# Performance work log

Hardware: AMD Instinct MI355X
Metric: run time of the kernel (lower is better)

The kernel has to match this reference:

```python
import jax, jax.numpy as jnp
import numpy as np


def setup_inputs() -> dict:
    key = jax.random.key(0)
    T, B, N = 2048, 16, 2048
    spikes = (jax.random.uniform(key, (T, B, N)) < 0.05).astype(jnp.float32)
    return {"input_spikes": spikes, "duration": 100}


def reference(input_spikes, duration):
    # Causal sliding-window (boxcar) sum over the time axis of length `duration`,
    # equivalent to conv1d with a ones kernel and causal padding, then clamp to [0,1].
    # psp[t] = clip( sum_{k=max(0,t-duration+1)}^{t} x[k], 0, 1 )
    T = input_spikes.shape[0]
    c = jnp.cumsum(input_spikes, axis=0)                     # [T, ...]
    pad = [(duration, 0)] + [(0, 0)] * (input_spikes.ndim - 1)
    c_shift = jnp.pad(c, pad)[:T]                            # c[t-duration], 0 for t<duration
    win = c - c_shift
    return jnp.clip(win, 0.0, 1.0)
```

## Files before the change

### kernel.cpp

```cpp
#include <hip/hip_runtime.h>


#define T_TOTAL 2048
#define M_COLS  (16 * 2048)
#define CHUNK   256
#define VEC     2
#define BATCH   8

typedef float v2f __attribute__((ext_vector_type(2)));

__device__ __forceinline__ void loadb(v2f (&dst)[BATCH], const v2f* __restrict__ xc,
                                      int tb, int stride) {
    #pragma unroll
    for (int i = 0; i < BATCH; ++i) dst[i] = xc[(tb + i) * stride];
}

__device__ __forceinline__ void procb(const v2f (&v)[BATCH], v2f* __restrict__ oc,
                                      int tb, int stride, int t0, int duration,
                                      int& last0, int& last1) {
    #pragma unroll
    for (int i = 0; i < BATCH; ++i) {
        const int tt = tb + i;
        if (v[i].x != 0.0f) last0 = tt;
        if (v[i].y != 0.0f) last1 = tt;
        if (tt >= t0) {
            v2f o;
            o.x = (tt - last0 < duration) ? 1.0f : 0.0f;
            o.y = (tt - last1 < duration) ? 1.0f : 0.0f;
            __builtin_nontemporal_store(o, &oc[tt * stride]);
        }
    }
}

__global__ __launch_bounds__(256, 1) void psp_scan_kernel(
    const float* __restrict__ x,
    const int*  __restrict__ dur_p,
    float* __restrict__ out)
{
    const int pair = blockIdx.x * blockDim.x + threadIdx.x;
    const int col  = pair * VEC;
    const int t0   = blockIdx.y * CHUNK;
    const int duration = dur_p[0];

    int hal = (duration - 1 + (BATCH - 1)) & ~(BATCH - 1);
    if (hal > t0) hal = t0;
    const int tstart = t0 - hal;
    const int NB = (hal + CHUNK) / BATCH;

    int last0 = tstart - duration;
    int last1 = last0;

    const v2f* __restrict__ xc = (const v2f*)(x + col);
    v2f* __restrict__ oc       = (v2f*)(out + col);
    const int stride = M_COLS / VEC;

    v2f va[BATCH], vb[BATCH];

    int t = tstart;
    loadb(va, xc, t, stride);

    int b = 0;
    while (b + 2 <= NB) {
        loadb(vb, xc, t + BATCH, stride);
        __builtin_amdgcn_sched_barrier(0);
        procb(va, oc, t, stride, t0, duration, last0, last1);

        if (b + 2 < NB) loadb(va, xc, t + 2 * BATCH, stride);
        __builtin_amdgcn_sched_barrier(0);
        procb(vb, oc, t + BATCH, stride, t0, duration, last0, last1);

        t += 2 * BATCH;
        b += 2;
    }
    if (b < NB) {
        procb(va, oc, t, stride, t0, duration, last0, last1);
    }
}

extern "C" void kernel_launch(void* const* d_in, const int* in_sizes, int n_in,
                              void* d_out, int out_size, void* d_ws, size_t ws_size,
                              hipStream_t stream) {
    const float* x     = (const float*)d_in[0];
    const int*   dur_p = (const int*)d_in[1];
    float*       out   = (float*)d_out;

    dim3 grid(M_COLS / VEC / 256, T_TOTAL / CHUNK);
    dim3 block(256);
    psp_scan_kernel<<<grid, block, 0, stream>>>(x, dur_p, out);
}
```

Measured before the change: 465.8 us.

## Halve time chunk, raise occupancy, replace double-buffering with inline-asm batched loads

Halves the time chunk per block, which doubles the grid, and raises launch bounds to allow 4 blocks per CU. Latency is meant to be hidden by occupancy instead of the software double-buffer, which is replaced by simple batched inline-asm loads followed by a full vmcnt wait. The halo warm-up is split into a separate loop without stores. Smaller chunks increase the relative halo reread overhead (about 104 extra rows per 128), adding memory traffic.

```diff
diff --git a/kernel.cpp b/kernel.cpp
--- a/kernel.cpp
+++ b/kernel.cpp
@@ -3,36 +3,16 @@
 
 #define T_TOTAL 2048
 #define M_COLS  (16 * 2048)
-#define CHUNK   256
+#define CHUNK   128
 #define VEC     2
 #define BATCH   8
 
 typedef float v2f __attribute__((ext_vector_type(2)));
 
-__device__ __forceinline__ void loadb(v2f (&dst)[BATCH], const v2f* __restrict__ xc,
-                                      int tb, int stride) {
-    #pragma unroll
-    for (int i = 0; i < BATCH; ++i) dst[i] = xc[(tb + i) * stride];
-}
+#define GLOAD2(dst, ptr) \
+    asm volatile("global_load_dwordx2 %0, %1, off" : "=v"(dst) : "v"(ptr))
 
-__device__ __forceinline__ void procb(const v2f (&v)[BATCH], v2f* __restrict__ oc,
-                                      int tb, int stride, int t0, int duration,
-                                      int& last0, int& last1) {
-    #pragma unroll
-    for (int i = 0; i < BATCH; ++i) {
-        const int tt = tb + i;
-        if (v[i].x != 0.0f) last0 = tt;
-        if (v[i].y != 0.0f) last1 = tt;
-        if (tt >= t0) {
-            v2f o;
-            o.x = (tt - last0 < duration) ? 1.0f : 0.0f;
-            o.y = (tt - last1 < duration) ? 1.0f : 0.0f;
-            __builtin_nontemporal_store(o, &oc[tt * stride]);
-        }
-    }
-}
-
-__global__ __launch_bounds__(256, 1) void psp_scan_kernel(
+__global__ __launch_bounds__(256, 4) void psp_scan_kernel(
     const float* __restrict__ x,
     const int*  __restrict__ dur_p,
     float* __restrict__ out)
@@ -45,7 +25,6 @@
     int hal = (duration - 1 + (BATCH - 1)) & ~(BATCH - 1);
     if (hal > t0) hal = t0;
     const int tstart = t0 - hal;
-    const int NB = (hal + CHUNK) / BATCH;
 
     int last0 = tstart - duration;
     int last1 = last0;
@@ -54,26 +33,37 @@
     v2f* __restrict__ oc       = (v2f*)(out + col);
     const int stride = M_COLS / VEC;
 
-    v2f va[BATCH], vb[BATCH];
+    v2f v[BATCH];
+    int t = tstart;
 
-    int t = tstart;
-    loadb(va, xc, t, stride);
+    for (; t < t0; t += BATCH) {
+        #pragma unroll
+        for (int i = 0; i < BATCH; ++i) GLOAD2(v[i], xc + (t + i) * stride);
+        asm volatile("s_waitcnt vmcnt(0)" ::: "memory");
+        __builtin_amdgcn_sched_barrier(0);
+        #pragma unroll
+        for (int i = 0; i < BATCH; ++i) {
+            const int tt = t + i;
+            if (v[i].x != 0.0f) last0 = tt;
+            if (v[i].y != 0.0f) last1 = tt;
+        }
+    }
 
-    int b = 0;
-    while (b + 2 <= NB) {
-        loadb(vb, xc, t + BATCH, stride);
+    for (; t < t0 + CHUNK; t += BATCH) {
+        #pragma unroll
+        for (int i = 0; i < BATCH; ++i) GLOAD2(v[i], xc + (t + i) * stride);
+        asm volatile("s_waitcnt vmcnt(0)" ::: "memory");
         __builtin_amdgcn_sched_barrier(0);
-        procb(va, oc, t, stride, t0, duration, last0, last1);
-
-        if (b + 2 < NB) loadb(va, xc, t + 2 * BATCH, stride);
-        __builtin_amdgcn_sched_barrier(0);
-        procb(vb, oc, t + BATCH, stride, t0, duration, last0, last1);
-
-        t += 2 * BATCH;
-        b += 2;
-    }
-    if (b < NB) {
-        procb(va, oc, t, stride, t0, duration, last0, last1);
+        #pragma unroll
+        for (int i = 0; i < BATCH; ++i) {
+            const int tt = t + i;
+            if (v[i].x != 0.0f) last0 = tt;
+            if (v[i].y != 0.0f) last1 = tt;
+            v2f o;
+            o.x = (tt - last0 < duration) ? 1.0f : 0.0f;
+            o.y = (tt - last1 < duration) ? 1.0f : 0.0f;
+            __builtin_nontemporal_store(o, &oc[tt * stride]);
+        }
     }
 }
 
```

Measured after the change: 468.3 us. About the same (+0.5%).
